# Kernel optimization log

Measured on AMD Instinct MI355X. Metric: run time of the kernel, lower is better.

The kernel has to match this reference:

```python
import jax, jax.numpy as jnp
import numpy as np
from jax import lax

B, C, N = 8, 3, 65536
NUM_POINTS = 1024


def setup_inputs() -> dict:
    key = jax.random.key(0)
    points = jax.random.normal(key, (B, C, N), dtype=jnp.float32)
    return {"points": points}


def furthest_point_sampling(xyz, num_points):
    # xyz: (B, N, 3) -> indices (B, num_points), int32
    b, n, _ = xyz.shape
    init_idx = jnp.zeros((b,), dtype=jnp.int32)  # CUDA FPS seeds with index 0
    init_dists = jnp.full((b, n), 1e10, dtype=xyz.dtype)

    def step(carry, _):
        dists, last_idx = carry
        last_pt = jnp.take_along_axis(xyz, last_idx[:, None, None], axis=1)  # (B,1,3)
        d = jnp.sum(jnp.square(xyz - last_pt), axis=-1)  # (B,N) squared dist to newest pt
        dists = jnp.minimum(dists, d)
        nxt = jnp.argmax(dists, axis=-1).astype(jnp.int32)
        return (dists, nxt), nxt

    (_, _), rest = lax.scan(step, (init_dists, init_idx), None, length=num_points - 1)
    # rest: (num_points-1, B) -> (B, num_points)
    idx = jnp.concatenate([init_idx[None, :], rest], axis=0).T
    return idx


def reference(points):
    # points: (B, 3, N), channels-first as in the torch module
    xyz = jnp.transpose(points, (0, 2, 1))  # (B, N, 3)
    idx = furthest_point_sampling(xyz, NUM_POINTS)  # (B, num_points)
    # fps_gather_by_index: gather along point axis of (B, 3, N)
    new_points = jnp.take_along_axis(points, idx[:, None, :], axis=2)  # (B, 3, num_points)
    return new_points
```

## Files before the change

### kernel.cpp

```cpp
#include <hip/hip_runtime.h>


namespace {

constexpr int kB = 8;
constexpr int kN = 65536;
constexpr int kNP = 1024;
constexpr int kPB = 16;
constexpr int kThreads = 256;
constexpr int kPPT = kN / (kPB * kThreads);
constexpr int kGrp = kPPT / 4;
constexpr int kWaves = kThreads / 64;
constexpr int kSlots = kPB * kWaves;
constexpr int kRgn = 4;
constexpr int kRgnStride = 2 * kSlots;
constexpr int kBatchStride = kRgn * kRgnStride;
constexpr int kBlocks = 256;

template <int CTRL>
__device__ __forceinline__ unsigned long long dpp_max_u64(unsigned long long k) {
  const int lo = (int)(unsigned)k;
  const int hi = (int)(unsigned)(k >> 32);
  const unsigned plo = (unsigned)__builtin_amdgcn_update_dpp(lo, lo, CTRL, 0xF, 0xF, false);
  const unsigned phi = (unsigned)__builtin_amdgcn_update_dpp(hi, hi, CTRL, 0xF, 0xF, false);
  const unsigned long long p = ((unsigned long long)phi << 32) | plo;
  return p > k ? p : k;
}

__device__ __forceinline__ unsigned long long readlane_u64(unsigned long long v, int l) {
  const unsigned lo = (unsigned)__builtin_amdgcn_readlane((int)(unsigned)v, l);
  const unsigned hi = (unsigned)__builtin_amdgcn_readlane((int)(unsigned)(v >> 32), l);
  return ((unsigned long long)hi << 32) | lo;
}

__device__ __forceinline__ unsigned long long u64max(unsigned long long a,
                                                     unsigned long long b) {
  return a > b ? a : b;
}

__device__ __forceinline__ unsigned long long load_l2(const unsigned long long* p) {
  unsigned long long v;
  asm volatile("global_load_dwordx2 %0, %1, off sc0\n\ts_waitcnt vmcnt(0)"
               : "=v"(v)
               : "v"(p)
               : "memory");
  return v;
}

__device__ __forceinline__ void store_l2(unsigned long long* p, unsigned long long v) {
  asm volatile("global_store_dwordx2 %0, %1, off sc0" ::"v"(p), "v"(v) : "memory");
}

__global__ __launch_bounds__(kThreads) void fps_kernel(const float* __restrict__ pts,
                                                       float* __restrict__ out,
                                                       unsigned long long* __restrict__ slots,
                                                       unsigned* __restrict__ ctrl) {
  const int tid = threadIdx.x;
  const int lane = tid & 63;
  const int wave = tid >> 6;

  __shared__ int s_batch, s_slice;
  __shared__ unsigned long long s_mail[2][3];
  __shared__ int s_hist[kNP];

  if (tid == 0) {
    unsigned xcc;
    asm volatile("s_getreg_b32 %0, hwreg(HW_REG_XCC_ID)" : "=s"(xcc));
    const int home = (int)(xcc & 7u);
    int batch = -1, slice = -1;
    const int pos = (int)atomicAdd(&ctrl[home], 1u);
    if (pos < kPB) {
      batch = home;
      slice = pos;
    }
    __hip_atomic_fetch_add(&ctrl[8], 1u, __ATOMIC_RELEASE, __HIP_MEMORY_SCOPE_AGENT);
    if (batch < 0) {
      while (__hip_atomic_load(&ctrl[8], __ATOMIC_ACQUIRE, __HIP_MEMORY_SCOPE_AGENT) <
             (unsigned)kBlocks) {
        __builtin_amdgcn_s_sleep(8);
      }
      int need = (int)atomicAdd(&ctrl[9], 1u);
      for (int j = 0; j < kB; ++j) {
        int have = (int)__hip_atomic_load(&ctrl[j], __ATOMIC_RELAXED, __HIP_MEMORY_SCOPE_AGENT);
        have = have > kPB ? kPB : have;
        const int vac = kPB - have;
        if (need < vac) {
          batch = j;
          slice = have + need;
          break;
        }
        need -= vac;
      }
    }
    s_batch = batch;
    s_slice = slice;
    s_mail[0][0] = s_mail[0][1] = s_mail[0][2] = 0xFFFFFFFF00000000ull;
    s_mail[1][0] = s_mail[1][1] = s_mail[1][2] = 0xFFFFFFFF00000000ull;
  }
  __syncthreads();

  const int batch = s_batch;
  const int slice = s_slice;
  if (batch < 0) return;

  const float* __restrict__ xb = pts + (size_t)batch * 3 * kN;
  const float* __restrict__ yb = xb + kN;
  const float* __restrict__ zb = xb + 2 * kN;

  const int sbase = slice * (kThreads * kPPT);
  const int base0 = sbase + tid * 4;
  float px[kPPT], py[kPPT], pz[kPPT], dist[kPPT];
#pragma unroll
  for (int g = 0; g < kGrp; ++g) {
    const int base = base0 + g * (kThreads * 4);
    const float4 vx = *reinterpret_cast<const float4*>(xb + base);
    const float4 vy = *reinterpret_cast<const float4*>(yb + base);
    const float4 vz = *reinterpret_cast<const float4*>(zb + base);
    px[g * 4 + 0] = vx.x; px[g * 4 + 1] = vx.y; px[g * 4 + 2] = vx.z; px[g * 4 + 3] = vx.w;
    py[g * 4 + 0] = vy.x; py[g * 4 + 1] = vy.y; py[g * 4 + 2] = vy.z; py[g * 4 + 3] = vy.w;
    pz[g * 4 + 0] = vz.x; pz[g * 4 + 1] = vz.y; pz[g * 4 + 2] = vz.z; pz[g * 4 + 3] = vz.w;
  }
#pragma unroll
  for (int k = 0; k < kPPT; ++k) dist[k] = 1e10f;

  float qx = xb[0], qy = yb[0], qz = zb[0];

  unsigned long long* const sb = slots + (size_t)batch * kBatchStride;
  const int slot = slice * kWaves + wave;

  for (int it = 1; it < kNP; ++it) {
    float bd = -1.0f;
    int bi = 0;
#pragma unroll
    for (int g = 0; g < kGrp; ++g) {
#pragma unroll
      for (int j = 0; j < 4; ++j) {
        const int k = g * 4 + j;
        const float dx = px[k] - qx;
        const float dy = py[k] - qy;
        const float dz = pz[k] - qz;
        const float ss =
            __fadd_rn(__fadd_rn(__fmul_rn(dx, dx), __fmul_rn(dy, dy)), __fmul_rn(dz, dz));
        const float nd = fminf(dist[k], ss);
        dist[k] = nd;
        if (nd > bd) {
          bd = nd;
          bi = base0 + g * (kThreads * 4) + j;
        }
      }
    }

    unsigned long long key = ((unsigned long long)__float_as_uint(bd) << 32) |
                             ((unsigned long long)(0xFFFFu - (unsigned)bi) << 16) |
                             (unsigned long long)(unsigned)it;

    key = dpp_max_u64<0x111>(key);
    key = dpp_max_u64<0x112>(key);
    key = dpp_max_u64<0x114>(key);
    key = dpp_max_u64<0x118>(key);
    key = dpp_max_u64<0x142>(key);
    key = dpp_max_u64<0x143>(key);

    unsigned long long* const rgn = sb + (size_t)(it & (kRgn - 1)) * kRgnStride;

    if (lane == 63) {
      store_l2(rgn + slot, key);
      __hip_atomic_store(rgn + kSlots + slot, key, __ATOMIC_RELAXED,
                         __HIP_MEMORY_SCOPE_AGENT);
    }

    if (wave == 0) {
      unsigned long long sv;
      int round = 0;
      for (;;) {
        unsigned long long a = load_l2(rgn + lane);
        bool ok = (unsigned)(a & 0xFFFFull) == (unsigned)it;
        if (round >= 2 && !ok) {
          const unsigned long long fb = __hip_atomic_load(
              rgn + kSlots + lane, __ATOMIC_RELAXED, __HIP_MEMORY_SCOPE_AGENT);
          if ((unsigned)(fb & 0xFFFFull) == (unsigned)it) {
            a = fb;
            ok = true;
          }
        }
        if (__all(ok)) {
          sv = a;
          break;
        }
        ++round;
      }

      const int cand = (int)(0xFFFFu - ((unsigned)(sv >> 16) & 0xFFFFu));
      const float gx = xb[cand];
      const float gy = yb[cand];
      const float gz = zb[cand];

      unsigned long long k2 = sv;
      k2 = dpp_max_u64<0xB1>(k2);
      k2 = dpp_max_u64<0x4E>(k2);
      k2 = dpp_max_u64<0x141>(k2);
      k2 = dpp_max_u64<0x140>(k2);
      const unsigned long long r0 = readlane_u64(k2, 0);
      const unsigned long long r1 = readlane_u64(k2, 16);
      const unsigned long long r2 = readlane_u64(k2, 32);
      const unsigned long long r3 = readlane_u64(k2, 48);
      const unsigned long long win = u64max(u64max(r0, r1), u64max(r2, r3));

      const unsigned long long m = __ballot(sv == win);
      const int src = (int)__ffsll(m) - 1;
      qx = __int_as_float(__builtin_amdgcn_readlane(__float_as_int(gx), src));
      qy = __int_as_float(__builtin_amdgcn_readlane(__float_as_int(gy), src));
      qz = __int_as_float(__builtin_amdgcn_readlane(__float_as_int(gz), src));

      if (lane == 0) {
        const int p = it & 1;
        const unsigned long long t = (unsigned long long)(unsigned)it << 32;
        __hip_atomic_store(&s_mail[p][0], t | (unsigned)__float_as_uint(qx),
                           __ATOMIC_RELAXED, __HIP_MEMORY_SCOPE_WORKGROUP);
        __hip_atomic_store(&s_mail[p][1], t | (unsigned)__float_as_uint(qy),
                           __ATOMIC_RELAXED, __HIP_MEMORY_SCOPE_WORKGROUP);
        __hip_atomic_store(&s_mail[p][2], t | (unsigned)__float_as_uint(qz),
                           __ATOMIC_RELAXED, __HIP_MEMORY_SCOPE_WORKGROUP);
        s_hist[it] = (int)(0xFFFFu - ((unsigned)(win >> 16) & 0xFFFFu));
      }
    } else {
      const int p = it & 1;
      unsigned long long w0, w1, w2;
      do {
        w0 = __hip_atomic_load(&s_mail[p][0], __ATOMIC_RELAXED, __HIP_MEMORY_SCOPE_WORKGROUP);
        w1 = __hip_atomic_load(&s_mail[p][1], __ATOMIC_RELAXED, __HIP_MEMORY_SCOPE_WORKGROUP);
        w2 = __hip_atomic_load(&s_mail[p][2], __ATOMIC_RELAXED, __HIP_MEMORY_SCOPE_WORKGROUP);
      } while (!((unsigned)(w0 >> 32) == (unsigned)it &&
                 (unsigned)(w1 >> 32) == (unsigned)it &&
                 (unsigned)(w2 >> 32) == (unsigned)it));
      qx = __int_as_float((int)(unsigned)w0);
      qy = __int_as_float((int)(unsigned)w1);
      qz = __int_as_float((int)(unsigned)w2);
    }
  }

  __syncthreads();

  if (slice == 0) {
    float* __restrict__ ob = out + (size_t)batch * 3 * kNP;
    for (int j = tid; j < kNP; j += kThreads) {
      const int id = (j == 0) ? 0 : s_hist[j];
      ob[j] = xb[id];
      ob[kNP + j] = yb[id];
      ob[2 * kNP + j] = zb[id];
    }
  }
}

}

extern "C" void kernel_launch(void* const* d_in, const int* in_sizes, int n_in,
                              void* d_out, int out_size, void* d_ws, size_t ws_size,
                              hipStream_t stream) {
  (void)in_sizes;
  (void)n_in;
  (void)out_size;
  (void)ws_size;
  const float* pts = (const float*)d_in[0];
  float* out = (float*)d_out;
  unsigned* ctrl = (unsigned*)d_ws;
  unsigned long long* slots = (unsigned long long*)((char*)d_ws + 1024);
  hipMemsetAsync(d_ws, 0, 64, stream);
  fps_kernel<<<dim3(kBlocks), dim3(kThreads), 0, stream>>>(pts, out, slots, ctrl);
}
```

Measured before the change: 1.769 ms.

## Reduce per-block wave keys in LDS before publishing one key per block

Each wave now posts its argmax key to shared memory, and wave 0 combines the four keys before writing a single key per block to the global exchange region. That cuts the global slots per batch from 64 to 16 and the ring grows from 4 to 16 regions. The final cross-block reduction works on 16 lanes, so it drops the readlane-based combine across 64 lanes. This adds an intra-block LDS spin on the critical path but removes global traffic and lowers the number of polled slots.

```diff
diff --git a/kernel.cpp b/kernel.cpp
--- a/kernel.cpp
+++ b/kernel.cpp
@@ -11,10 +11,8 @@
 constexpr int kPPT = kN / (kPB * kThreads);
 constexpr int kGrp = kPPT / 4;
 constexpr int kWaves = kThreads / 64;
-constexpr int kSlots = kPB * kWaves;
-constexpr int kRgn = 4;
-constexpr int kRgnStride = 2 * kSlots;
-constexpr int kBatchStride = kRgn * kRgnStride;
+constexpr int kRgn = 16;
+constexpr int kRgnStride = 32;
 constexpr int kBlocks = 256;
 
 template <int CTRL>
@@ -27,17 +25,6 @@
   return p > k ? p : k;
 }
 
-__device__ __forceinline__ unsigned long long readlane_u64(unsigned long long v, int l) {
-  const unsigned lo = (unsigned)__builtin_amdgcn_readlane((int)(unsigned)v, l);
-  const unsigned hi = (unsigned)__builtin_amdgcn_readlane((int)(unsigned)(v >> 32), l);
-  return ((unsigned long long)hi << 32) | lo;
-}
-
-__device__ __forceinline__ unsigned long long u64max(unsigned long long a,
-                                                     unsigned long long b) {
-  return a > b ? a : b;
-}
-
 __device__ __forceinline__ unsigned long long load_l2(const unsigned long long* p) {
   unsigned long long v;
   asm volatile("global_load_dwordx2 %0, %1, off sc0\n\ts_waitcnt vmcnt(0)"
@@ -60,6 +47,7 @@
   const int wave = tid >> 6;
 
   __shared__ int s_batch, s_slice;
+  __shared__ unsigned long long s_wkey[kWaves];
   __shared__ unsigned long long s_mail[2][3];
   __shared__ int s_hist[kNP];
 
@@ -94,6 +82,7 @@
     }
     s_batch = batch;
     s_slice = slice;
+    s_wkey[0] = s_wkey[1] = s_wkey[2] = s_wkey[3] = 0xFFFFull;
     s_mail[0][0] = s_mail[0][1] = s_mail[0][2] = 0xFFFFFFFF00000000ull;
     s_mail[1][0] = s_mail[1][1] = s_mail[1][2] = 0xFFFFFFFF00000000ull;
   }
@@ -125,8 +114,7 @@
 
   float qx = xb[0], qy = yb[0], qz = zb[0];
 
-  unsigned long long* const sb = slots + (size_t)batch * kBatchStride;
-  const int slot = slice * kWaves + wave;
+  unsigned long long* const sb = slots + (size_t)batch * kRgn * kRgnStride;
 
   for (int it = 1; it < kNP; ++it) {
     float bd = -1.0f;
@@ -161,23 +149,35 @@
     key = dpp_max_u64<0x142>(key);
     key = dpp_max_u64<0x143>(key);
 
-    unsigned long long* const rgn = sb + (size_t)(it & (kRgn - 1)) * kRgnStride;
-
     if (lane == 63) {
-      store_l2(rgn + slot, key);
-      __hip_atomic_store(rgn + kSlots + slot, key, __ATOMIC_RELAXED,
-                         __HIP_MEMORY_SCOPE_AGENT);
+      __hip_atomic_store(&s_wkey[wave], key, __ATOMIC_RELAXED, __HIP_MEMORY_SCOPE_WORKGROUP);
     }
 
     if (wave == 0) {
+      unsigned long long bk;
+      for (;;) {
+        bk = __hip_atomic_load(&s_wkey[lane & (kWaves - 1)], __ATOMIC_RELAXED,
+                               __HIP_MEMORY_SCOPE_WORKGROUP);
+        if (__all((unsigned)(bk & 0xFFFFull) == (unsigned)it)) break;
+      }
+      bk = dpp_max_u64<0xB1>(bk);
+      bk = dpp_max_u64<0x4E>(bk);
+
+      unsigned long long* const rgn = sb + (size_t)(it & (kRgn - 1)) * kRgnStride;
+      if (lane == 0) {
+        store_l2(rgn + slice, bk);
+        __hip_atomic_store(rgn + kPB + slice, bk, __ATOMIC_RELAXED,
+                           __HIP_MEMORY_SCOPE_AGENT);
+      }
+
       unsigned long long sv;
       int round = 0;
       for (;;) {
-        unsigned long long a = load_l2(rgn + lane);
+        unsigned long long a = load_l2(rgn + (lane & (kPB - 1)));
         bool ok = (unsigned)(a & 0xFFFFull) == (unsigned)it;
         if (round >= 2 && !ok) {
           const unsigned long long fb = __hip_atomic_load(
-              rgn + kSlots + lane, __ATOMIC_RELAXED, __HIP_MEMORY_SCOPE_AGENT);
+              rgn + kPB + (lane & (kPB - 1)), __ATOMIC_RELAXED, __HIP_MEMORY_SCOPE_AGENT);
           if ((unsigned)(fb & 0xFFFFull) == (unsigned)it) {
             a = fb;
             ok = true;
@@ -200,13 +200,8 @@
       k2 = dpp_max_u64<0x4E>(k2);
       k2 = dpp_max_u64<0x141>(k2);
       k2 = dpp_max_u64<0x140>(k2);
-      const unsigned long long r0 = readlane_u64(k2, 0);
-      const unsigned long long r1 = readlane_u64(k2, 16);
-      const unsigned long long r2 = readlane_u64(k2, 32);
-      const unsigned long long r3 = readlane_u64(k2, 48);
-      const unsigned long long win = u64max(u64max(r0, r1), u64max(r2, r3));
-
-      const unsigned long long m = __ballot(sv == win);
+
+      const unsigned long long m = __ballot(sv == k2);
       const int src = (int)__ffsll(m) - 1;
       qx = __int_as_float(__builtin_amdgcn_readlane(__float_as_int(gx), src));
       qy = __int_as_float(__builtin_amdgcn_readlane(__float_as_int(gy), src));
@@ -221,7 +216,7 @@
                            __ATOMIC_RELAXED, __HIP_MEMORY_SCOPE_WORKGROUP);
         __hip_atomic_store(&s_mail[p][2], t | (unsigned)__float_as_uint(qz),
                            __ATOMIC_RELAXED, __HIP_MEMORY_SCOPE_WORKGROUP);
-        s_hist[it] = (int)(0xFFFFu - ((unsigned)(win >> 16) & 0xFFFFu));
+        s_hist[it] = (int)(0xFFFFu - ((unsigned)(k2 >> 16) & 0xFFFFu));
       }
     } else {
       const int p = it & 1;
```

Result: faster. 1.429 ms, median of 2 (-19.2%).
